# Optimization experiments

Measured on AMD Instinct MI355X. Metric: run time of the kernel, lower is better.

Reference implementation:

```python
import jax, jax.numpy as jnp
import numpy as np

EPS = 1e-9


def setup_inputs() -> dict:
    key = jax.random.key(0)
    kE, kQ, kK, kV = jax.random.split(key, 4)
    B, S, D = 8, 2048, 256
    return {
        "E": jax.random.normal(kE, (B, S, D), dtype=jnp.float32),
        "WQ": jax.random.normal(kQ, (D, D), dtype=jnp.float32) * (1.0 / np.sqrt(D)),
        "WK": jax.random.normal(kK, (D, D), dtype=jnp.float32) * (1.0 / np.sqrt(D)),
        "WV": jax.random.normal(kV, (D, D), dtype=jnp.float32) * (1.0 / np.sqrt(D)),
    }


def reference(E, WQ, WK, WV):
    # E: [B, S, D]; WQ/WK/WV: [D, D] (torch Linear weight, applied as x @ W.T)
    D = E.shape[-1]
    scale = jnp.asarray(np.sqrt(D), dtype=E.dtype)
    Q = jnp.einsum('bsd,ed->bse', E, WQ)
    K = jnp.einsum('bsd,ed->bse', E, WK)
    V = jnp.einsum('bsd,ed->bse', E, WV)
    # Full score matrix [B, S, S] (non-flash, as in the original)
    W = jnp.einsum('bqd,bkd->bqk', Q, K) / scale
    # mask=True path: causal tril mask, additionally zeroed where W == 0 exactly
    S_len = W.shape[-1]
    tril = jnp.tril(jnp.ones((S_len, S_len), dtype=W.dtype))  # [S, S]
    M = jnp.where(W == 0, jnp.zeros_like(W), tril[None, :, :])
    # custom masked softmax with epsilon denominator
    x_max = jnp.max(W, axis=-1, keepdims=True)
    x_exp = jnp.exp(W - x_max) * M
    A = x_exp / (jnp.sum(x_exp, axis=-1, keepdims=True) + EPS)
    return jnp.einsum('bqk,bkd->bqd', A, V)
```

## Files before the change

### kernel.cpp

```cpp
#include <hip/hip_runtime.h>
#include <stdint.h>


typedef __attribute__((ext_vector_type(8)))  short bf16x8;
typedef __attribute__((ext_vector_type(4)))  float f32x4;
typedef __attribute__((ext_vector_type(16))) float f32x16;

#define NEGF  -3.0e38f
#define MINIT -1.0e30f

__device__ __forceinline__ unsigned short f2bf(float f){
  union { float f; unsigned u; } v; v.f = f;
  unsigned r = v.u + 0x7FFFu + ((v.u >> 16) & 1u);
  return (unsigned short)(r >> 16);
}
__device__ __forceinline__ unsigned pk2(float a, float b){
  return (unsigned)f2bf(a) | ((unsigned)f2bf(b) << 16);
}
__device__ __forceinline__ float bf2f(unsigned short h){
  union { unsigned u; float f; } v; v.u = ((unsigned)h) << 16; return v.f;
}

__global__ void wconv_kernel(const float* __restrict__ WQ, const float* __restrict__ WK,
                             const float* __restrict__ WV, unsigned short* __restrict__ Wb)
{
  const int widx = blockIdx.x, kk = blockIdx.y, n = threadIdx.x;
  const float* W = (widx==0) ? WQ : ((widx==1) ? WK : WV);
  unsigned short* dst = Wb + (size_t)widx*65536 + kk*8192 + n*32;
#pragma unroll
  for (int gp=0; gp<4; ++gp){
    const int g = gp ^ (n & 3);
    const float* src = W + (size_t)n*256 + kk*32 + g*8;
    float4 a = *reinterpret_cast<const float4*>(src);
    float4 c = *reinterpret_cast<const float4*>(src + 4);
    uint4 v; v.x = pk2(a.x,a.y); v.y = pk2(a.z,a.w); v.z = pk2(c.x,c.y); v.w = pk2(c.z,c.w);
    *reinterpret_cast<uint4*>(dst + gp*8) = v;
  }
}

__global__ __launch_bounds__(256, 3) void qkv_proj_kernel(
    const float* __restrict__ E, const unsigned short* __restrict__ Wb,
    unsigned short* __restrict__ Qb, unsigned short* __restrict__ Ka,
    unsigned short* __restrict__ Vf)
{
  __shared__ unsigned short As[32*256];
  __shared__ unsigned short Bs[2][8192];

  const int m0 = blockIdx.x * 32;
  const int b  = m0 >> 11;
  const int sb = m0 & 2047;
  const int t = threadIdx.x, lane = t & 63, w = t >> 6;
  const int hi = lane >> 4, lo = lane & 15;

  auto stageB = [&](int widx, int kk, int buf){
    const char* src = (const char*)Wb + widx*131072 + kk*16384;
    char* dst = (char*)Bs[buf];
#pragma unroll
    for (int c=0;c<4;c++){
      const int off = c*4096 + t*16;
      __builtin_amdgcn_global_load_lds(
        (const __attribute__((address_space(1))) unsigned int*)(src + off),
        (__attribute__((address_space(3))) unsigned int*)(dst + off), 16, 0, 0);
    }
  };

  stageB(0, 0, 0);
  {
    const int r = t >> 3, c0 = (t & 7) * 32;
    const float* ga = E + (size_t)(m0 + r)*256 + c0;
#pragma unroll
    for (int gg=0; gg<4; ++gg){
      float4 x = *reinterpret_cast<const float4*>(ga + gg*8);
      float4 y = *reinterpret_cast<const float4*>(ga + gg*8 + 4);
      uint4 v; v.x = pk2(x.x,x.y); v.y = pk2(x.z,x.w); v.z = pk2(y.x,y.y); v.w = pk2(y.z,y.w);
      const int g = (t & 7)*4 + gg;
      *reinterpret_cast<uint4*>((char*)As + r*512 + ((g ^ (r & 7)) << 4)) = v;
    }
  }

  const f32x4 fzero = {0.f,0.f,0.f,0.f};
  const int u = sb >> 5;
  for (int widx=0; widx<3; ++widx){
    f32x4 acc[2][4];
#pragma unroll
    for (int mi=0;mi<2;mi++)
#pragma unroll
      for (int f=0;f<4;f++) acc[mi][f] = fzero;
    if (widx) stageB(widx, 0, 0);

    for (int kk=0; kk<8; ++kk){
      const int bb = kk & 1;
      if (kk < 7) stageB(widx, kk+1, bb^1);
      if (kk < 7) asm volatile("s_waitcnt vmcnt(4) lgkmcnt(0)" ::: "memory");
      else        asm volatile("s_waitcnt vmcnt(0) lgkmcnt(0)" ::: "memory");
      __builtin_amdgcn_sched_barrier(0);
      __builtin_amdgcn_s_barrier();
      __builtin_amdgcn_sched_barrier(0);

      bf16x8 afr[2], bfr[4];
#pragma unroll
      for (int mi=0;mi<2;mi++){
        const int r = mi*16 + lo;
        afr[mi] = *reinterpret_cast<const bf16x8*>(
            (const char*)As + r*512 + (((kk*4 + hi) ^ (r & 7)) << 4));
      }
#pragma unroll
      for (int f=0;f<4;f++){
        const int n = w*64 + f*16 + lo;
        bfr[f] = *reinterpret_cast<const bf16x8*>(
            (const char*)Bs[bb] + n*64 + ((hi ^ (n & 3)) << 4));
      }
#pragma unroll
      for (int mi=0;mi<2;mi++)
#pragma unroll
        for (int f=0;f<4;f++)
          acc[mi][f] = __builtin_amdgcn_mfma_f32_16x16x32_bf16(afr[mi], bfr[f], acc[mi][f], 0,0,0);

      asm volatile("s_waitcnt lgkmcnt(0)" ::: "memory");
      __builtin_amdgcn_sched_barrier(0);
      __builtin_amdgcn_s_barrier();
    }

    if (widx == 0){
#pragma unroll
      for (int mi=0;mi<2;mi++)
#pragma unroll
        for (int f=0;f<4;f++){
          const int col = w*64 + f*16 + lo;
#pragma unroll
          for (int r=0;r<4;r++)
            Qb[(size_t)(m0 + mi*16 + hi*4 + r)*256 + col] = f2bf(acc[mi][f][r]*0.0625f);
        }
    } else if (widx == 1){
      unsigned short* Kab = Ka + (size_t)b*524288 + (size_t)u*8192;
#pragma unroll
      for (int mi=0;mi<2;mi++)
#pragma unroll
        for (int f=0;f<4;f++){
          const int c = w*4 + f;
          const int j = lo & 7;
          const int lb = 32*(lo>>3) + mi*16 + hi*4;
#pragma unroll
          for (int r=0;r<4;r++)
            Kab[(size_t)(c*64 + lb + r)*8 + j] = f2bf(acc[mi][f][r]);
        }
    } else {
      unsigned short* Vfb = Vf + (size_t)b*524288;
#pragma unroll
      for (int mi=0;mi<2;mi++)
#pragma unroll
        for (int f=0;f<4;f++){
          const int d  = w*64 + f*16 + lo;
          const int dt = d >> 5;
          const int l  = 32*(hi&1) + (d&31);
          const int j0 = 4*(hi>>1);
          unsigned short* vp = Vfb + ((size_t)((u*2 + mi)*8 + dt)*64 + l)*8 + j0;
          uint2 pw; pw.x = pk2(acc[mi][f][0], acc[mi][f][1]);
          pw.y = pk2(acc[mi][f][2], acc[mi][f][3]);
          *reinterpret_cast<uint2*>(vp) = pw;
        }
    }
  }
}

__global__ __launch_bounds__(256, 2) void attn_kernel(
    const unsigned short* __restrict__ Qb, const unsigned short* __restrict__ Ka,
    const unsigned short* __restrict__ Vf, float* __restrict__ Out,
    const int sched, unsigned short* __restrict__ Pb, float* __restrict__ ML)
{
  __shared__ char Lds[2][32768];

  const int bid  = blockIdx.x;
  const int b    = bid & 7;
  const int slot = bid >> 3;
  int tau, chunk, mode, u0, u1;
  if (sched){
    tau = 31 - (slot >> 1); chunk = slot & 1;
    u0 = chunk ? (tau + 1) : 0;
    u1 = chunk ? (2*tau + 2) : (tau + 1);
    mode = 1 + chunk;
  } else {
    tau = 31 - slot; chunk = 0; u0 = 0; u1 = 2*tau + 2; mode = 0;
  }
  const int Qbase = tau * 64;

  const int t = threadIdx.x;
  const int lane = t & 63, w = t >> 6;
  const int qs = w >> 1, dh = w & 1;
  const int l31 = lane & 31, h5 = lane >> 5;
  const int q_l = Qbase + qs*32 + l31;
  const int diagu = 2*tau + qs;

  const char* Kab = (const char*)Ka + (size_t)b*1048576;
  const char* Vfb = (const char*)Vf + (size_t)b*1048576;

  auto stage = [&](int uu, int buf){
    const char* gk = Kab + (size_t)uu*16384;
    const char* gv = Vfb + (size_t)uu*16384;
    char* lk = Lds[buf];
    char* lv = Lds[buf] + 16384;
#pragma unroll
    for (int i=0;i<4;i++){
      const int off = i*4096 + t*16;
      __builtin_amdgcn_global_load_lds(
        (const __attribute__((address_space(1))) unsigned int*)(gk + off),
        (__attribute__((address_space(3))) unsigned int*)(lk + off), 16, 0, 0);
      __builtin_amdgcn_global_load_lds(
        (const __attribute__((address_space(1))) unsigned int*)(gv + off),
        (__attribute__((address_space(3))) unsigned int*)(lv + off), 16, 0, 0);
    }
  };

  bf16x8 qf[16];
  {
    const unsigned short* Qp = Qb + ((size_t)(b*2048 + q_l))*256 + h5*8;
#pragma unroll
    for (int c=0;c<16;c++) qf[c] = *reinterpret_cast<const bf16x8*>(Qp + c*16);
  }

  const f32x16 z16 = {0.f,0.f,0.f,0.f,0.f,0.f,0.f,0.f,0.f,0.f,0.f,0.f,0.f,0.f,0.f,0.f};
  f32x16 accO[4];
#pragma unroll
  for (int i=0;i<4;i++) accO[i] = z16;
  float m_run = MINIT, l_run = 0.f;

  stage(u0, 0);
  if (u0 + 1 < u1) stage(u0 + 1, 1);

  for (int u = u0; u < u1; ++u){
    const int buf = (u - u0) & 1;
    if (u + 1 < u1) asm volatile("s_waitcnt vmcnt(8)" ::: "memory");
    else            asm volatile("s_waitcnt vmcnt(0)" ::: "memory");
    __builtin_amdgcn_sched_barrier(0);
    __builtin_amdgcn_s_barrier();
    __builtin_amdgcn_sched_barrier(0);

    const char* kt = Lds[buf];
    const char* lv = Lds[buf] + 16384 + dh*4096 + lane*16;

    f32x16 sv0 = z16, sv1 = z16;
#pragma unroll
    for (int c=0;c<16;c+=2){
      bf16x8 a0 = *reinterpret_cast<const bf16x8*>(kt + c*1024 + lane*16);
      bf16x8 a1 = *reinterpret_cast<const bf16x8*>(kt + (c+1)*1024 + lane*16);
      sv0 = __builtin_amdgcn_mfma_f32_32x32x16_bf16(a0, qf[c],   sv0, 0,0,0);
      sv1 = __builtin_amdgcn_mfma_f32_32x32x16_bf16(a1, qf[c+1], sv1, 0,0,0);
    }
    f32x16 s16 = sv0 + sv1;

    bf16x8 vf0[4], vf1[4];
#pragma unroll
    for (int i=0;i<4;i++){
      vf0[i] = *reinterpret_cast<const bf16x8*>(lv + i*1024);
      vf1[i] = *reinterpret_cast<const bf16x8*>(lv + 8192 + i*1024);
    }

    if (u >= diagu){
      const int kvb = u*32 + 4*h5;
#pragma unroll
      for (int r=0;r<16;r++){
        const int kv = kvb + (r&3) + 8*(r>>2);
        if (kv > q_l) s16[r] = NEGF;
      }
    }

    float t8[8], t4[4];
#pragma unroll
    for (int i=0;i<8;i++) t8[i] = fmaxf(s16[i], s16[i+8]);
#pragma unroll
    for (int i=0;i<4;i++) t4[i] = fmaxf(t8[i], t8[i+4]);
    float pmax = fmaxf(fmaxf(t4[0],t4[1]), fmaxf(t4[2],t4[3]));
    pmax = fmaxf(pmax, __shfl_xor(pmax, 32, 64));

    if (!__all(pmax - m_run <= 8.0f)){
      const float mn = fmaxf(m_run, pmax);
      const float alpha = __expf(m_run - mn);
#pragma unroll
      for (int i=0;i<4;i++) accO[i] *= alpha;
      l_run *= alpha;
      m_run = mn;
    }
    float p[16];
#pragma unroll
    for (int r=0;r<16;r++) p[r] = __expf(s16[r] - m_run);
#pragma unroll
    for (int i=0;i<8;i++) t8[i] = p[i] + p[i+8];
#pragma unroll
    for (int i=0;i<4;i++) t4[i] = t8[i] + t8[i+4];
    float ls = (t4[0]+t4[1]) + (t4[2]+t4[3]);
    ls += __shfl_xor(ls, 32, 64);
    l_run += ls;

    union { bf16x8 v; unsigned u32[4]; } pa0, pa1;
#pragma unroll
    for (int k=0;k<4;k++){
      pa0.u32[k] = pk2(p[2*k],   p[2*k+1]);
      pa1.u32[k] = pk2(p[8+2*k], p[9+2*k]);
    }

#pragma unroll
    for (int i=0;i<4;i++){
      accO[i] = __builtin_amdgcn_mfma_f32_32x32x16_bf16(vf0[i], pa0.v, accO[i], 0,0,0);
      accO[i] = __builtin_amdgcn_mfma_f32_32x32x16_bf16(vf1[i], pa1.v, accO[i], 0,0,0);
    }

    asm volatile("s_waitcnt lgkmcnt(0)" ::: "memory");
    __builtin_amdgcn_sched_barrier(0);
    __builtin_amdgcn_s_barrier();
    if (u + 2 < u1) stage(u + 2, buf);
  }

  if (mode && dh == 0 && lane < 32){
    float* mlp = ML + ((size_t)(((b*32 + tau)*2 + chunk)*64 + qs*32 + lane))*2;
    mlp[0] = m_run; mlp[1] = l_run;
  }

  const float inv = (mode == 0) ? 1.0f/(l_run + 1e-9f) : 1.0f;
  float* Tw = (float*)(&Lds[0][0]) + w*2048;
  const int qloc = lane >> 1, dc = (lane & 1) * 16;
#pragma unroll
  for (int i=0;i<4;i++){
#pragma unroll
    for (int r=0;r<16;r++)
      Tw[l31*33 + ((r&3) + 8*(r>>2) + 4*h5)] = accO[i][r] * inv;
    asm volatile("s_waitcnt lgkmcnt(0)" ::: "memory");
    __builtin_amdgcn_sched_barrier(0);
    const float* srcT = &Tw[qloc*33 + dc];
    if (mode < 2){
      float* dst = Out + ((size_t)(b*2048 + Qbase + qs*32 + qloc))*256 + dh*128 + i*32 + dc;
#pragma unroll
      for (int k=0;k<4;k++){
        float4 vv = { srcT[4*k], srcT[4*k+1], srcT[4*k+2], srcT[4*k+3] };
        *reinterpret_cast<float4*>(dst + 4*k) = vv;
      }
    } else {
      unsigned short* pb = Pb + (((size_t)(b*32 + tau)*64 + qs*32 + qloc))*256
                              + dh*128 + i*32 + dc;
      uint4 w0, w1;
      w0.x = pk2(srcT[0],  srcT[1]);  w0.y = pk2(srcT[2],  srcT[3]);
      w0.z = pk2(srcT[4],  srcT[5]);  w0.w = pk2(srcT[6],  srcT[7]);
      w1.x = pk2(srcT[8],  srcT[9]);  w1.y = pk2(srcT[10], srcT[11]);
      w1.z = pk2(srcT[12], srcT[13]); w1.w = pk2(srcT[14], srcT[15]);
      *reinterpret_cast<uint4*>(pb)     = w0;
      *reinterpret_cast<uint4*>(pb + 8) = w1;
    }
    asm volatile("s_waitcnt lgkmcnt(0)" ::: "memory");
    __builtin_amdgcn_sched_barrier(0);
  }
}

__global__ void combine_kernel(float* __restrict__ Out, const unsigned short* __restrict__ Pb,
                               const float* __restrict__ ML)
{
  const int b = blockIdx.x & 7, tt = blockIdx.x >> 3;
  const int t = threadIdx.x;
  const int q = t >> 2, dg = (t & 3) * 64;
  const float* mlp = ML + ((size_t)((b*32 + tt)*2)*64)*2;
  const float m0 = mlp[q*2],            l0 = mlp[q*2 + 1];
  const float m1 = mlp[(64 + q)*2],     l1 = mlp[(64 + q)*2 + 1];
  const float M  = fmaxf(m0, m1);
  const float e0 = __expf(m0 - M), e1 = __expf(m1 - M);
  const float inv = 1.0f/(e0*l0 + e1*l1 + 1e-9f);
  float* O = Out + ((size_t)(b*2048 + tt*64 + q))*256 + dg;
  const unsigned short* P = Pb + ((size_t)((b*32 + tt)*64 + q))*256 + dg;
#pragma unroll
  for (int k=0;k<8;k++){
    float4 a0 = *reinterpret_cast<const float4*>(O + 8*k);
    float4 a1 = *reinterpret_cast<const float4*>(O + 8*k + 4);
    uint4 pv = *reinterpret_cast<const uint4*>(P + 8*k);
    const unsigned short* us = (const unsigned short*)&pv;
    float4 o0, o1;
    o0.x = (e0*a0.x + e1*bf2f(us[0]))*inv; o0.y = (e0*a0.y + e1*bf2f(us[1]))*inv;
    o0.z = (e0*a0.z + e1*bf2f(us[2]))*inv; o0.w = (e0*a0.w + e1*bf2f(us[3]))*inv;
    o1.x = (e0*a1.x + e1*bf2f(us[4]))*inv; o1.y = (e0*a1.y + e1*bf2f(us[5]))*inv;
    o1.z = (e0*a1.z + e1*bf2f(us[6]))*inv; o1.w = (e0*a1.w + e1*bf2f(us[7]))*inv;
    *reinterpret_cast<float4*>(O + 8*k)     = o0;
    *reinterpret_cast<float4*>(O + 8*k + 4) = o1;
  }
}

extern "C" void kernel_launch(void* const* d_in, const int* in_sizes, int n_in,
                              void* d_out, int out_size, void* d_ws, size_t ws_size,
                              hipStream_t stream)
{
  const float* E  = (const float*)d_in[0];
  const float* WQ = (const float*)d_in[1];
  const float* WK = (const float*)d_in[2];
  const float* WV = (const float*)d_in[3];
  const size_t elems = (size_t)8*2048*256;

  unsigned short* Qb = (unsigned short*)d_ws;
  unsigned short* Ka = Qb + elems;
  unsigned short* Vf = Ka + elems;
  unsigned short* Wb = Vf + elems;
  const size_t base = 3*elems*2 + 393216;

  const size_t PB = (size_t)8*32*64*256*2;
  const size_t MLSZ = (size_t)8*32*2*64*2*4;
  if (ws_size < base) return;
  const int sched = (ws_size >= base + PB + MLSZ) ? 1 : 0;
  unsigned short* Pb = (unsigned short*)((char*)d_ws + base);
  float* ML = (float*)((char*)d_ws + base + PB);

  wconv_kernel<<<dim3(3,8), 256, 0, stream>>>(WQ, WK, WV, Wb);
  qkv_proj_kernel<<<512, 256, 0, stream>>>(E, Wb, Qb, Ka, Vf);
  attn_kernel<<<sched ? 512 : 256, 256, 0, stream>>>(Qb, Ka, Vf, (float*)d_out, sched, Pb, ML);
  if (sched) combine_kernel<<<256, 256, 0, stream>>>((float*)d_out, Pb, ML);
}
```

Baseline: 89.19 us.

## Split attention KV tiles across waves with LDS merge; widen QKV k-steps

The attention kernel now assigns alternating KV tiles to wave pairs, so each wave computes the full 256-wide output for its query strip. V is read straight from global memory instead of being staged in LDS. The two waves' partial softmax states are merged through shared memory at the end, and the chunk schedule is reordered to interleave heavy and light query tiles. The QKV projection stages 64-wide K slices per barrier and prefetches the next weight's first slice, at the cost of higher LDS use and lower occupancy. Risks include doubled accumulator registers (8 f32x16) and uncached V reads from global memory.

Result: slower. 111.7 us (+25.2%).

```diff
diff --git a/kernel.cpp b/kernel.cpp
--- a/kernel.cpp
+++ b/kernel.cpp
@@ -5,6 +5,7 @@
 typedef __attribute__((ext_vector_type(8)))  short bf16x8;
 typedef __attribute__((ext_vector_type(4)))  float f32x4;
 typedef __attribute__((ext_vector_type(16))) float f32x16;
+typedef __attribute__((ext_vector_type(4)))  unsigned int u32x4;
 
 #define NEGF  -3.0e38f
 #define MINIT -1.0e30f
@@ -38,25 +39,26 @@
   }
 }
 
-__global__ __launch_bounds__(256, 3) void qkv_proj_kernel(
+__global__ __launch_bounds__(256, 2) void qkv_proj_kernel(
     const float* __restrict__ E, const unsigned short* __restrict__ Wb,
     unsigned short* __restrict__ Qb, unsigned short* __restrict__ Ka,
     unsigned short* __restrict__ Vf)
 {
   __shared__ unsigned short As[32*256];
-  __shared__ unsigned short Bs[2][8192];
+  __shared__ unsigned short Bs[2][16384];
 
   const int m0 = blockIdx.x * 32;
   const int b  = m0 >> 11;
   const int sb = m0 & 2047;
+  const int u  = sb >> 5;
   const int t = threadIdx.x, lane = t & 63, w = t >> 6;
   const int hi = lane >> 4, lo = lane & 15;
 
-  auto stageB = [&](int widx, int kk, int buf){
-    const char* src = (const char*)Wb + widx*131072 + kk*16384;
+  auto stageB = [&](int widx, int kk2, int buf){
+    const char* src = (const char*)Wb + widx*131072 + kk2*32768;
     char* dst = (char*)Bs[buf];
 #pragma unroll
-    for (int c=0;c<4;c++){
+    for (int c=0;c<8;c++){
       const int off = c*4096 + t*16;
       __builtin_amdgcn_global_load_lds(
         (const __attribute__((address_space(1))) unsigned int*)(src + off),
@@ -79,46 +81,46 @@
   }
 
   const f32x4 fzero = {0.f,0.f,0.f,0.f};
-  const int u = sb >> 5;
   for (int widx=0; widx<3; ++widx){
     f32x4 acc[2][4];
 #pragma unroll
     for (int mi=0;mi<2;mi++)
 #pragma unroll
       for (int f=0;f<4;f++) acc[mi][f] = fzero;
-    if (widx) stageB(widx, 0, 0);
-
-    for (int kk=0; kk<8; ++kk){
-      const int bb = kk & 1;
-      if (kk < 7) stageB(widx, kk+1, bb^1);
-      if (kk < 7) asm volatile("s_waitcnt vmcnt(4) lgkmcnt(0)" ::: "memory");
-      else        asm volatile("s_waitcnt vmcnt(0) lgkmcnt(0)" ::: "memory");
+
+    for (int kk2=0; kk2<4; ++kk2){
+      const int bb = kk2 & 1;
+      asm volatile("s_waitcnt vmcnt(0) lgkmcnt(0)" ::: "memory");
       __builtin_amdgcn_sched_barrier(0);
       __builtin_amdgcn_s_barrier();
       __builtin_amdgcn_sched_barrier(0);
-
-      bf16x8 afr[2], bfr[4];
-#pragma unroll
-      for (int mi=0;mi<2;mi++){
-        const int r = mi*16 + lo;
-        afr[mi] = *reinterpret_cast<const bf16x8*>(
-            (const char*)As + r*512 + (((kk*4 + hi) ^ (r & 7)) << 4));
-      }
-#pragma unroll
-      for (int f=0;f<4;f++){
-        const int n = w*64 + f*16 + lo;
-        bfr[f] = *reinterpret_cast<const bf16x8*>(
-            (const char*)Bs[bb] + n*64 + ((hi ^ (n & 3)) << 4));
-      }
-#pragma unroll
-      for (int mi=0;mi<2;mi++)
-#pragma unroll
-        for (int f=0;f<4;f++)
-          acc[mi][f] = __builtin_amdgcn_mfma_f32_16x16x32_bf16(afr[mi], bfr[f], acc[mi][f], 0,0,0);
-
-      asm volatile("s_waitcnt lgkmcnt(0)" ::: "memory");
-      __builtin_amdgcn_sched_barrier(0);
-      __builtin_amdgcn_s_barrier();
+      if (kk2 < 3)      stageB(widx, kk2+1, bb^1);
+      else if (widx<2)  stageB(widx+1, 0, 0);
+
+      bf16x8 afr[2][2], bfr[4][2];
+#pragma unroll
+      for (int h=0;h<2;h++){
+        const int kh = kk2*2 + h;
+#pragma unroll
+        for (int mi=0;mi<2;mi++){
+          const int r = mi*16 + lo;
+          afr[mi][h] = *reinterpret_cast<const bf16x8*>(
+              (const char*)As + r*512 + (((kh*4 + hi) ^ (r & 7)) << 4));
+        }
+#pragma unroll
+        for (int f=0;f<4;f++){
+          const int n = w*64 + f*16 + lo;
+          bfr[f][h] = *reinterpret_cast<const bf16x8*>(
+              (const char*)Bs[bb] + h*16384 + n*64 + ((hi ^ (n & 3)) << 4));
+        }
+      }
+#pragma unroll
+      for (int h=0;h<2;h++)
+#pragma unroll
+        for (int mi=0;mi<2;mi++)
+#pragma unroll
+          for (int f=0;f<4;f++)
+            acc[mi][f] = __builtin_amdgcn_mfma_f32_16x16x32_bf16(afr[mi][h], bfr[f][h], acc[mi][f], 0,0,0);
     }
 
     if (widx == 0){
@@ -168,25 +170,24 @@
     const unsigned short* __restrict__ Vf, float* __restrict__ Out,
     const int sched, unsigned short* __restrict__ Pb, float* __restrict__ ML)
 {
-  __shared__ char Lds[2][32768];
-
-  const int bid  = blockIdx.x;
-  const int b    = bid & 7;
-  const int slot = bid >> 3;
+  __shared__ char Kt[4][16384];
+  __shared__ float Msh[2][2][32];
+  __shared__ float Lsh[2][2][32];
+
+  const int bid = blockIdx.x, b = bid & 7, slot = bid >> 3;
   int tau, chunk, mode, u0, u1;
   if (sched){
-    tau = 31 - (slot >> 1); chunk = slot & 1;
+    const int ts = slot >> 1; chunk = slot & 1;
+    tau = (ts < 16) ? (31 - ts) : (ts - 16);
     u0 = chunk ? (tau + 1) : 0;
     u1 = chunk ? (2*tau + 2) : (tau + 1);
     mode = 1 + chunk;
-  } else {
-    tau = 31 - slot; chunk = 0; u0 = 0; u1 = 2*tau + 2; mode = 0;
-  }
+  } else { tau = 31 - slot; chunk = 0; u0 = 0; u1 = 2*tau + 2; mode = 0; }
   const int Qbase = tau * 64;
 
   const int t = threadIdx.x;
   const int lane = t & 63, w = t >> 6;
-  const int qs = w >> 1, dh = w & 1;
+  const int qs = w >> 1, ks = w & 1;
   const int l31 = lane & 31, h5 = lane >> 5;
   const int q_l = Qbase + qs*32 + l31;
   const int diagu = 2*tau + qs;
@@ -195,19 +196,14 @@
   const char* Vfb = (const char*)Vf + (size_t)b*1048576;
 
   auto stage = [&](int uu, int buf){
-    const char* gk = Kab + (size_t)uu*16384;
-    const char* gv = Vfb + (size_t)uu*16384;
-    char* lk = Lds[buf];
-    char* lv = Lds[buf] + 16384;
+    const char* src = Kab + (size_t)uu*16384;
+    char* dstl = (char*)Kt[buf];
 #pragma unroll
     for (int i=0;i<4;i++){
       const int off = i*4096 + t*16;
       __builtin_amdgcn_global_load_lds(
-        (const __attribute__((address_space(1))) unsigned int*)(gk + off),
-        (__attribute__((address_space(3))) unsigned int*)(lk + off), 16, 0, 0);
-      __builtin_amdgcn_global_load_lds(
-        (const __attribute__((address_space(1))) unsigned int*)(gv + off),
-        (__attribute__((address_space(3))) unsigned int*)(lv + off), 16, 0, 0);
+        (const __attribute__((address_space(1))) unsigned int*)(src + off),
+        (__attribute__((address_space(3))) unsigned int*)(dstl + off), 16, 0, 0);
     }
   };
 
@@ -219,133 +215,136 @@
   }
 
   const f32x16 z16 = {0.f,0.f,0.f,0.f,0.f,0.f,0.f,0.f,0.f,0.f,0.f,0.f,0.f,0.f,0.f,0.f};
-  f32x16 accO[4];
-#pragma unroll
-  for (int i=0;i<4;i++) accO[i] = z16;
+  f32x16 accO[8];
+#pragma unroll
+  for (int i=0;i<8;i++) accO[i] = z16;
   float m_run = MINIT, l_run = 0.f;
 
   stage(u0, 0);
   if (u0 + 1 < u1) stage(u0 + 1, 1);
 
-  for (int u = u0; u < u1; ++u){
-    const int buf = (u - u0) & 1;
-    if (u + 1 < u1) asm volatile("s_waitcnt vmcnt(8)" ::: "memory");
-    else            asm volatile("s_waitcnt vmcnt(0)" ::: "memory");
+  const int npair = (u1 - u0 + 1) >> 1;
+  for (int p = 0; p < npair; ++p){
+    const int base = u0 + 2*p;
+    asm volatile("s_waitcnt vmcnt(0) lgkmcnt(0)" ::: "memory");
     __builtin_amdgcn_sched_barrier(0);
     __builtin_amdgcn_s_barrier();
     __builtin_amdgcn_sched_barrier(0);
-
-    const char* kt = Lds[buf];
-    const char* lv = Lds[buf] + 16384 + dh*4096 + lane*16;
-
-    f32x16 sv0 = z16, sv1 = z16;
-#pragma unroll
-    for (int c=0;c<16;c+=2){
-      bf16x8 a0 = *reinterpret_cast<const bf16x8*>(kt + c*1024 + lane*16);
-      bf16x8 a1 = *reinterpret_cast<const bf16x8*>(kt + (c+1)*1024 + lane*16);
-      sv0 = __builtin_amdgcn_mfma_f32_32x32x16_bf16(a0, qf[c],   sv0, 0,0,0);
-      sv1 = __builtin_amdgcn_mfma_f32_32x32x16_bf16(a1, qf[c+1], sv1, 0,0,0);
-    }
-    f32x16 s16 = sv0 + sv1;
-
-    bf16x8 vf0[4], vf1[4];
-#pragma unroll
-    for (int i=0;i<4;i++){
-      vf0[i] = *reinterpret_cast<const bf16x8*>(lv + i*1024);
-      vf1[i] = *reinterpret_cast<const bf16x8*>(lv + 8192 + i*1024);
-    }
-
-    if (u >= diagu){
-      const int kvb = u*32 + 4*h5;
-#pragma unroll
-      for (int r=0;r<16;r++){
-        const int kv = kvb + (r&3) + 8*(r>>2);
-        if (kv > q_l) s16[r] = NEGF;
-      }
-    }
-
-    float t8[8], t4[4];
-#pragma unroll
-    for (int i=0;i<8;i++) t8[i] = fmaxf(s16[i], s16[i+8]);
-#pragma unroll
-    for (int i=0;i<4;i++) t4[i] = fmaxf(t8[i], t8[i+4]);
-    float pmax = fmaxf(fmaxf(t4[0],t4[1]), fmaxf(t4[2],t4[3]));
-    pmax = fmaxf(pmax, __shfl_xor(pmax, 32, 64));
-
-    if (!__all(pmax - m_run <= 8.0f)){
-      const float mn = fmaxf(m_run, pmax);
-      const float alpha = __expf(m_run - mn);
-#pragma unroll
-      for (int i=0;i<4;i++) accO[i] *= alpha;
-      l_run *= alpha;
-      m_run = mn;
-    }
-    float p[16];
-#pragma unroll
-    for (int r=0;r<16;r++) p[r] = __expf(s16[r] - m_run);
-#pragma unroll
-    for (int i=0;i<8;i++) t8[i] = p[i] + p[i+8];
-#pragma unroll
-    for (int i=0;i<4;i++) t4[i] = t8[i] + t8[i+4];
-    float ls = (t4[0]+t4[1]) + (t4[2]+t4[3]);
-    ls += __shfl_xor(ls, 32, 64);
-    l_run += ls;
-
-    union { bf16x8 v; unsigned u32[4]; } pa0, pa1;
-#pragma unroll
-    for (int k=0;k<4;k++){
-      pa0.u32[k] = pk2(p[2*k],   p[2*k+1]);
-      pa1.u32[k] = pk2(p[8+2*k], p[9+2*k]);
-    }
-
-#pragma unroll
-    for (int i=0;i<4;i++){
-      accO[i] = __builtin_amdgcn_mfma_f32_32x32x16_bf16(vf0[i], pa0.v, accO[i], 0,0,0);
-      accO[i] = __builtin_amdgcn_mfma_f32_32x32x16_bf16(vf1[i], pa1.v, accO[i], 0,0,0);
-    }
-
-    asm volatile("s_waitcnt lgkmcnt(0)" ::: "memory");
-    __builtin_amdgcn_sched_barrier(0);
-    __builtin_amdgcn_s_barrier();
-    if (u + 2 < u1) stage(u + 2, buf);
-  }
-
-  if (mode && dh == 0 && lane < 32){
-    float* mlp = ML + ((size_t)(((b*32 + tau)*2 + chunk)*64 + qs*32 + lane))*2;
-    mlp[0] = m_run; mlp[1] = l_run;
-  }
-
-  const float inv = (mode == 0) ? 1.0f/(l_run + 1e-9f) : 1.0f;
-  float* Tw = (float*)(&Lds[0][0]) + w*2048;
-  const int qloc = lane >> 1, dc = (lane & 1) * 16;
-#pragma unroll
-  for (int i=0;i<4;i++){
-#pragma unroll
-    for (int r=0;r<16;r++)
-      Tw[l31*33 + ((r&3) + 8*(r>>2) + 4*h5)] = accO[i][r] * inv;
-    asm volatile("s_waitcnt lgkmcnt(0)" ::: "memory");
-    __builtin_amdgcn_sched_barrier(0);
-    const float* srcT = &Tw[qloc*33 + dc];
-    if (mode < 2){
-      float* dst = Out + ((size_t)(b*2048 + Qbase + qs*32 + qloc))*256 + dh*128 + i*32 + dc;
+    const int nb = ((p + 1) & 1) * 2;
+    if (base + 2 < u1) stage(base + 2, nb);
+    if (base + 3 < u1) stage(base + 3, nb + 1);
+
+    const int myu = base + ks;
+    if (myu < u1){
+      const char* kt = Kt[(p & 1)*2 + ks];
+      f32x16 sv0 = z16, sv1 = z16;
+#pragma unroll
+      for (int c=0;c<16;c+=2){
+        bf16x8 a0 = *reinterpret_cast<const bf16x8*>(kt + c*1024 + lane*16);
+        bf16x8 a1 = *reinterpret_cast<const bf16x8*>(kt + (c+1)*1024 + lane*16);
+        sv0 = __builtin_amdgcn_mfma_f32_32x32x16_bf16(a0, qf[c],   sv0, 0,0,0);
+        sv1 = __builtin_amdgcn_mfma_f32_32x32x16_bf16(a1, qf[c+1], sv1, 0,0,0);
+      }
+      f32x16 s16v = sv0 + sv1;
+
+      if (myu >= diagu){
+        const int kvb = myu*32 + 4*h5;
+#pragma unroll
+        for (int r=0;r<16;r++){
+          const int kv = kvb + (r&3) + 8*(r>>2);
+          if (kv > q_l) s16v[r] = NEGF;
+        }
+      }
+
+      float t8[8], t4[4];
+#pragma unroll
+      for (int i=0;i<8;i++) t8[i] = fmaxf(s16v[i], s16v[i+8]);
+#pragma unroll
+      for (int i=0;i<4;i++) t4[i] = fmaxf(t8[i], t8[i+4]);
+      float pmax = fmaxf(fmaxf(t4[0],t4[1]), fmaxf(t4[2],t4[3]));
+      pmax = fmaxf(pmax, __shfl_xor(pmax, 32, 64));
+
+      if (!__all(pmax - m_run <= 8.0f)){
+        const float mn = fmaxf(m_run, pmax);
+        const float alpha = __expf(m_run - mn);
+#pragma unroll
+        for (int i=0;i<8;i++) accO[i] *= alpha;
+        l_run *= alpha;
+        m_run = mn;
+      }
+      float pv[16];
+#pragma unroll
+      for (int r=0;r<16;r++) pv[r] = __expf(s16v[r] - m_run);
+#pragma unroll
+      for (int i=0;i<8;i++) t8[i] = pv[i] + pv[i+8];
+#pragma unroll
+      for (int i=0;i<4;i++) t4[i] = t8[i] + t8[i+4];
+      float ls = (t4[0]+t4[1]) + (t4[2]+t4[3]);
+      ls += __shfl_xor(ls, 32, 64);
+      l_run += ls;
+
+      union { bf16x8 v; unsigned u32[4]; } pa0, pa1;
 #pragma unroll
       for (int k=0;k<4;k++){
-        float4 vv = { srcT[4*k], srcT[4*k+1], srcT[4*k+2], srcT[4*k+3] };
-        *reinterpret_cast<float4*>(dst + 4*k) = vv;
-      }
+        pa0.u32[k] = pk2(pv[2*k],   pv[2*k+1]);
+        pa1.u32[k] = pk2(pv[8+2*k], pv[9+2*k]);
+      }
+
+      const char* Vu = Vfb + (size_t)myu*16384 + lane*16;
+#pragma unroll
+      for (int i=0;i<8;i++){
+        bf16x8 va = *reinterpret_cast<const bf16x8*>(Vu + i*1024);
+        bf16x8 vb = *reinterpret_cast<const bf16x8*>(Vu + 8192 + i*1024);
+        accO[i] = __builtin_amdgcn_mfma_f32_32x32x16_bf16(va, pa0.v, accO[i], 0,0,0);
+        accO[i] = __builtin_amdgcn_mfma_f32_32x32x16_bf16(vb, pa1.v, accO[i], 0,0,0);
+      }
+    }
+  }
+
+  if (lane < 32){ Msh[qs][ks][l31] = m_run; Lsh[qs][ks][l31] = l_run; }
+  __syncthreads();
+  const float m0j = Msh[qs][0][l31], m1j = Msh[qs][1][l31];
+  const float l0j = Lsh[qs][0][l31], l1j = Lsh[qs][1][l31];
+  const float Mj = fmaxf(m0j, m1j);
+  const float e0 = __expf(m0j - Mj), e1 = __expf(m1j - Mj);
+  const float Lj = e0*l0j + e1*l1j;
+  const float inv = (mode == 0) ? 1.0f/(Lj + 1e-9f) : 1.0f;
+  const float sca = (ks ? e1 : e0) * inv;
+  if (mode && ks == 0 && lane < 32){
+    float* mlp = ML + ((size_t)((b*32 + tau)*2 + chunk)*64 + qs*32 + l31)*2;
+    mlp[0] = Mj; mlp[1] = Lj;
+  }
+  __syncthreads();
+
+  float* T = (float*)(&Kt[0][0]);
+  const int qp = t >> 2, ql = qp & 31, qss = qp >> 5;
+  const int d8 = (t & 3) * 8;
+#pragma unroll
+  for (int i=0;i<8;i++){
+#pragma unroll
+    for (int r=0;r<16;r++){
+      const int dl = (r&3) + 8*(r>>2) + 4*h5;
+      T[((qs*2 + ks)*32 + l31)*33 + dl] = accO[i][r] * sca;
+    }
+    __syncthreads();
+    const float* Ta = T + ((qss*2 + 0)*32 + ql)*33 + d8;
+    const float* Tb = T + ((qss*2 + 1)*32 + ql)*33 + d8;
+    float o[8];
+#pragma unroll
+    for (int j=0;j<8;j++) o[j] = Ta[j] + Tb[j];
+    if (mode <= 1){
+      float* dst = Out + ((size_t)(b*2048 + Qbase + qp))*256 + i*32 + d8;
+      f32x4 v0 = {o[0],o[1],o[2],o[3]}, v1 = {o[4],o[5],o[6],o[7]};
+      *reinterpret_cast<f32x4*>(dst)     = v0;
+      *reinterpret_cast<f32x4*>(dst + 4) = v1;
     } else {
-      unsigned short* pb = Pb + (((size_t)(b*32 + tau)*64 + qs*32 + qloc))*256
-                              + dh*128 + i*32 + dc;
-      uint4 w0, w1;
-      w0.x = pk2(srcT[0],  srcT[1]);  w0.y = pk2(srcT[2],  srcT[3]);
-      w0.z = pk2(srcT[4],  srcT[5]);  w0.w = pk2(srcT[6],  srcT[7]);
-      w1.x = pk2(srcT[8],  srcT[9]);  w1.y = pk2(srcT[10], srcT[11]);
-      w1.z = pk2(srcT[12], srcT[13]); w1.w = pk2(srcT[14], srcT[15]);
-      *reinterpret_cast<uint4*>(pb)     = w0;
-      *reinterpret_cast<uint4*>(pb + 8) = w1;
-    }
-    asm volatile("s_waitcnt lgkmcnt(0)" ::: "memory");
-    __builtin_amdgcn_sched_barrier(0);
+      unsigned short* pb = Pb + ((size_t)((b*32 + tau)*64 + qp))*256 + i*32 + d8;
+      u32x4 wv;
+      wv.x = pk2(o[0],o[1]); wv.y = pk2(o[2],o[3]);
+      wv.z = pk2(o[4],o[5]); wv.w = pk2(o[6],o[7]);
+      *reinterpret_cast<u32x4*>(pb) = wv;
+    }
+    __syncthreads();
   }
 }
 
@@ -356,8 +355,8 @@
   const int t = threadIdx.x;
   const int q = t >> 2, dg = (t & 3) * 64;
   const float* mlp = ML + ((size_t)((b*32 + tt)*2)*64)*2;
-  const float m0 = mlp[q*2],            l0 = mlp[q*2 + 1];
-  const float m1 = mlp[(64 + q)*2],     l1 = mlp[(64 + q)*2 + 1];
+  const float m0 = mlp[q*2],        l0 = mlp[q*2 + 1];
+  const float m1 = mlp[(64+q)*2],   l1 = mlp[(64+q)*2 + 1];
   const float M  = fmaxf(m0, m1);
   const float e0 = __expf(m0 - M), e1 = __expf(m1 - M);
   const float inv = 1.0f/(e0*l0 + e1*l1 + 1e-9f);
@@ -367,8 +366,8 @@
   for (int k=0;k<8;k++){
     float4 a0 = *reinterpret_cast<const float4*>(O + 8*k);
     float4 a1 = *reinterpret_cast<const float4*>(O + 8*k + 4);
-    uint4 pv = *reinterpret_cast<const uint4*>(P + 8*k);
-    const unsigned short* us = (const unsigned short*)&pv;
+    uint4 pvv = *reinterpret_cast<const uint4*>(P + 8*k);
+    const unsigned short* us = (const unsigned short*)&pvv;
     float4 o0, o1;
     o0.x = (e0*a0.x + e1*bf2f(us[0]))*inv; o0.y = (e0*a0.y + e1*bf2f(us[1]))*inv;
     o0.z = (e0*a0.z + e1*bf2f(us[2]))*inv; o0.w = (e0*a0.w + e1*bf2f(us[3]))*inv;
```

## Pre-swizzle weights into MFMA fragment order and load directly from global

Applied to the files above, without the earlier changes.

The weight conversion kernel now writes bf16 weights in per-lane MFMA fragment order, so the projection kernel loads B fragments straight from global/L2 instead of staging through double-buffered LDS with barriers. This removes LDS traffic and per-iteration block syncs and raises occupancy (launch bounds 4), at the cost of more global/L2 loads per wave. The attention schedule also reorders query tiles so heavy and light tiles interleave across block slots, for better load balance.

Result: slower. 91.46 us (+2.6%).

```diff
diff --git a/kernel.cpp b/kernel.cpp
--- a/kernel.cpp
+++ b/kernel.cpp
@@ -5,6 +5,7 @@
 typedef __attribute__((ext_vector_type(8)))  short bf16x8;
 typedef __attribute__((ext_vector_type(4)))  float f32x4;
 typedef __attribute__((ext_vector_type(16))) float f32x16;
+typedef __attribute__((ext_vector_type(4)))  unsigned int u32x4;
 
 #define NEGF  -3.0e38f
 #define MINIT -1.0e30f
@@ -22,49 +23,37 @@
 }
 
 __global__ void wconv_kernel(const float* __restrict__ WQ, const float* __restrict__ WK,
-                             const float* __restrict__ WV, unsigned short* __restrict__ Wb)
-{
-  const int widx = blockIdx.x, kk = blockIdx.y, n = threadIdx.x;
+                             const float* __restrict__ WV, unsigned short* __restrict__ Wf)
+{
+  const int widx = blockIdx.x, kk = blockIdx.y;
+  const int t = threadIdx.x;
+  const int nb = t >> 4, lo = t & 15;
   const float* W = (widx==0) ? WQ : ((widx==1) ? WK : WV);
-  unsigned short* dst = Wb + (size_t)widx*65536 + kk*8192 + n*32;
-#pragma unroll
-  for (int gp=0; gp<4; ++gp){
-    const int g = gp ^ (n & 3);
-    const float* src = W + (size_t)n*256 + kk*32 + g*8;
-    float4 a = *reinterpret_cast<const float4*>(src);
-    float4 c = *reinterpret_cast<const float4*>(src + 4);
+  const float* src = W + (size_t)(nb*16 + lo)*256 + kk*32;
+  unsigned short* dst = Wf + (((size_t)(widx*8 + kk)*16 + nb)*64)*8;
+#pragma unroll
+  for (int hi=0; hi<4; ++hi){
+    float4 a = *reinterpret_cast<const float4*>(src + hi*8);
+    float4 c = *reinterpret_cast<const float4*>(src + hi*8 + 4);
     uint4 v; v.x = pk2(a.x,a.y); v.y = pk2(a.z,a.w); v.z = pk2(c.x,c.y); v.w = pk2(c.z,c.w);
-    *reinterpret_cast<uint4*>(dst + gp*8) = v;
-  }
-}
-
-__global__ __launch_bounds__(256, 3) void qkv_proj_kernel(
-    const float* __restrict__ E, const unsigned short* __restrict__ Wb,
+    *reinterpret_cast<uint4*>(dst + ((size_t)(hi*16 + lo))*8) = v;
+  }
+}
+
+__global__ __launch_bounds__(256, 4) void qkv_proj_kernel(
+    const float* __restrict__ E, const unsigned short* __restrict__ Wf,
     unsigned short* __restrict__ Qb, unsigned short* __restrict__ Ka,
     unsigned short* __restrict__ Vf)
 {
   __shared__ unsigned short As[32*256];
-  __shared__ unsigned short Bs[2][8192];
 
   const int m0 = blockIdx.x * 32;
   const int b  = m0 >> 11;
   const int sb = m0 & 2047;
+  const int u  = sb >> 5;
   const int t = threadIdx.x, lane = t & 63, w = t >> 6;
   const int hi = lane >> 4, lo = lane & 15;
 
-  auto stageB = [&](int widx, int kk, int buf){
-    const char* src = (const char*)Wb + widx*131072 + kk*16384;
-    char* dst = (char*)Bs[buf];
-#pragma unroll
-    for (int c=0;c<4;c++){
-      const int off = c*4096 + t*16;
-      __builtin_amdgcn_global_load_lds(
-        (const __attribute__((address_space(1))) unsigned int*)(src + off),
-        (__attribute__((address_space(3))) unsigned int*)(dst + off), 16, 0, 0);
-    }
-  };
-
-  stageB(0, 0, 0);
   {
     const int r = t >> 3, c0 = (t & 7) * 32;
     const float* ga = E + (size_t)(m0 + r)*256 + c0;
@@ -77,27 +66,26 @@
       *reinterpret_cast<uint4*>((char*)As + r*512 + ((g ^ (r & 7)) << 4)) = v;
     }
   }
+  __syncthreads();
 
   const f32x4 fzero = {0.f,0.f,0.f,0.f};
-  const int u = sb >> 5;
+  const char* Wfb = (const char*)Wf;
+
   for (int widx=0; widx<3; ++widx){
     f32x4 acc[2][4];
 #pragma unroll
     for (int mi=0;mi<2;mi++)
 #pragma unroll
       for (int f=0;f<4;f++) acc[mi][f] = fzero;
-    if (widx) stageB(widx, 0, 0);
-
+
+#pragma unroll 2
     for (int kk=0; kk<8; ++kk){
-      const int bb = kk & 1;
-      if (kk < 7) stageB(widx, kk+1, bb^1);
-      if (kk < 7) asm volatile("s_waitcnt vmcnt(4) lgkmcnt(0)" ::: "memory");
-      else        asm volatile("s_waitcnt vmcnt(0) lgkmcnt(0)" ::: "memory");
-      __builtin_amdgcn_sched_barrier(0);
-      __builtin_amdgcn_s_barrier();
-      __builtin_amdgcn_sched_barrier(0);
-
-      bf16x8 afr[2], bfr[4];
+      const char* wp = Wfb + ((size_t)((widx*8 + kk)*16 + w*4))*1024 + lane*16;
+      bf16x8 bfr[4];
+#pragma unroll
+      for (int f=0;f<4;f++)
+        bfr[f] = *reinterpret_cast<const bf16x8*>(wp + f*1024);
+      bf16x8 afr[2];
 #pragma unroll
       for (int mi=0;mi<2;mi++){
         const int r = mi*16 + lo;
@@ -105,20 +93,10 @@
             (const char*)As + r*512 + (((kk*4 + hi) ^ (r & 7)) << 4));
       }
 #pragma unroll
-      for (int f=0;f<4;f++){
-        const int n = w*64 + f*16 + lo;
-        bfr[f] = *reinterpret_cast<const bf16x8*>(
-            (const char*)Bs[bb] + n*64 + ((hi ^ (n & 3)) << 4));
-      }
-#pragma unroll
       for (int mi=0;mi<2;mi++)
 #pragma unroll
         for (int f=0;f<4;f++)
           acc[mi][f] = __builtin_amdgcn_mfma_f32_16x16x32_bf16(afr[mi], bfr[f], acc[mi][f], 0,0,0);
-
-      asm volatile("s_waitcnt lgkmcnt(0)" ::: "memory");
-      __builtin_amdgcn_sched_barrier(0);
-      __builtin_amdgcn_s_barrier();
     }
 
     if (widx == 0){
@@ -175,7 +153,8 @@
   const int slot = bid >> 3;
   int tau, chunk, mode, u0, u1;
   if (sched){
-    tau = 31 - (slot >> 1); chunk = slot & 1;
+    const int ts = slot >> 1; chunk = slot & 1;
+    tau = (ts < 16) ? (31 - ts) : (ts - 16);
     u0 = chunk ? (tau + 1) : 0;
     u1 = chunk ? (2*tau + 2) : (tau + 1);
     mode = 1 + chunk;
@@ -336,13 +315,13 @@
     } else {
       unsigned short* pb = Pb + (((size_t)(b*32 + tau)*64 + qs*32 + qloc))*256
                               + dh*128 + i*32 + dc;
-      uint4 w0, w1;
+      u32x4 w0, w1;
       w0.x = pk2(srcT[0],  srcT[1]);  w0.y = pk2(srcT[2],  srcT[3]);
       w0.z = pk2(srcT[4],  srcT[5]);  w0.w = pk2(srcT[6],  srcT[7]);
       w1.x = pk2(srcT[8],  srcT[9]);  w1.y = pk2(srcT[10], srcT[11]);
       w1.z = pk2(srcT[12], srcT[13]); w1.w = pk2(srcT[14], srcT[15]);
-      *reinterpret_cast<uint4*>(pb)     = w0;
-      *reinterpret_cast<uint4*>(pb + 8) = w1;
+      *reinterpret_cast<u32x4*>(pb)     = w0;
+      *reinterpret_cast<u32x4*>(pb + 8) = w1;
     }
     asm volatile("s_waitcnt lgkmcnt(0)" ::: "memory");
     __builtin_amdgcn_sched_barrier(0);
@@ -356,8 +335,8 @@
   const int t = threadIdx.x;
   const int q = t >> 2, dg = (t & 3) * 64;
   const float* mlp = ML + ((size_t)((b*32 + tt)*2)*64)*2;
-  const float m0 = mlp[q*2],            l0 = mlp[q*2 + 1];
-  const float m1 = mlp[(64 + q)*2],     l1 = mlp[(64 + q)*2 + 1];
+  const float m0 = mlp[q*2],        l0 = mlp[q*2 + 1];
+  const float m1 = mlp[(64+q)*2],   l1 = mlp[(64+q)*2 + 1];
   const float M  = fmaxf(m0, m1);
   const float e0 = __expf(m0 - M), e1 = __expf(m1 - M);
   const float inv = 1.0f/(e0*l0 + e1*l1 + 1e-9f);
@@ -367,8 +346,8 @@
   for (int k=0;k<8;k++){
     float4 a0 = *reinterpret_cast<const float4*>(O + 8*k);
     float4 a1 = *reinterpret_cast<const float4*>(O + 8*k + 4);
-    uint4 pv = *reinterpret_cast<const uint4*>(P + 8*k);
-    const unsigned short* us = (const unsigned short*)&pv;
+    uint4 pvv = *reinterpret_cast<const uint4*>(P + 8*k);
+    const unsigned short* us = (const unsigned short*)&pvv;
     float4 o0, o1;
     o0.x = (e0*a0.x + e1*bf2f(us[0]))*inv; o0.y = (e0*a0.y + e1*bf2f(us[1]))*inv;
     o0.z = (e0*a0.z + e1*bf2f(us[2]))*inv; o0.w = (e0*a0.w + e1*bf2f(us[3]))*inv;
@@ -392,7 +371,7 @@
   unsigned short* Qb = (unsigned short*)d_ws;
   unsigned short* Ka = Qb + elems;
   unsigned short* Vf = Ka + elems;
-  unsigned short* Wb = Vf + elems;
+  unsigned short* Wf = Vf + elems;
   const size_t base = 3*elems*2 + 393216;
 
   const size_t PB = (size_t)8*32*64*256*2;
@@ -402,8 +381,8 @@
   unsigned short* Pb = (unsigned short*)((char*)d_ws + base);
   float* ML = (float*)((char*)d_ws + base + PB);
 
-  wconv_kernel<<<dim3(3,8), 256, 0, stream>>>(WQ, WK, WV, Wb);
-  qkv_proj_kernel<<<512, 256, 0, stream>>>(E, Wb, Qb, Ka, Vf);
+  wconv_kernel<<<dim3(3,8), 256, 0, stream>>>(WQ, WK, WV, Wf);
+  qkv_proj_kernel<<<512, 256, 0, stream>>>(E, Wf, Qb, Ka, Vf);
   attn_kernel<<<sched ? 512 : 256, 256, 0, stream>>>(Qb, Ka, Vf, (float*)d_out, sched, Pb, ML);
   if (sched) combine_kernel<<<256, 256, 0, stream>>>((float*)d_out, Pb, ML);
 }
```
